# Kernel tuning notes

Hardware: AMD Instinct MI355X
Metric: run time of the kernel (lower is better)

The kernel has to match this reference:

```python
import jax, jax.numpy as jnp
import numpy as np
from jax.scipy.linalg import expm as _expm

B, D = 1024, 128
_SQRT3 = 3.0 ** 0.5
_C1, _C2 = 0.5 - _SQRT3 / 6.0, 0.5 + _SQRT3 / 6.0


def setup_inputs() -> dict:
    key = jax.random.key(0)
    k_t, k_y, k_a, k_w = jax.random.split(key, 4)
    scale = 1.0 / np.sqrt(D)  # keep ||Omega|| moderate so expm is well-conditioned
    return {
        "t0": jax.random.uniform(k_t, (B,), dtype=jnp.float32),
        "h": jnp.float32(0.1),
        "y0": jax.random.normal(k_y, (B, D), dtype=jnp.float32),
        "A0": jax.random.normal(k_a, (B, D, D), dtype=jnp.float32) * scale,
        "W": jax.random.normal(k_w, (B, D, D), dtype=jnp.float32) * scale,
    }


def reference(t0, h, y0, A0, W):
    # A(t) = A0 + t * W evaluated at the two Gauss-Legendre nodes
    t1 = t0 + _C1 * h  # (B,)
    t2 = t0 + _C2 * h  # (B,)
    A1 = A0 + t1[:, None, None] * W  # (B, D, D)
    A2 = A0 + t2[:, None, None] * W  # (B, D, D)
    alpha1 = (h * 0.5) * (A1 + A2)
    alpha2 = (h * _SQRT3) * (A2 - A1)
    comm = alpha1 @ alpha2 - alpha2 @ alpha1  # [alpha1, alpha2]
    Omega = alpha1 - comm / 12.0
    U = jax.vmap(_expm)(Omega)  # batched matrix exponential (B, D, D)
    y_next = jnp.einsum("bij,bj->bi", U, y0)  # (B, D)
    return y_next, jnp.stack((A1, A2), axis=0)
```

## Files before the change

kernel.cpp:

```cpp
#include <hip/hip_runtime.h>

#define B_SZ 1024
#define D_SZ 128
#define KTERMS 7
#define QPAD 36

typedef float vfloat4 __attribute__((ext_vector_type(4)));

__device__ inline float bflo(unsigned u) { return __uint_as_float(u << 16); }
__device__ inline float bfhi(unsigned u) { return __uint_as_float(u & 0xffff0000u); }

__device__ inline void dot32x2(const unsigned* ra, const unsigned* rw,
                               const float* v, float& oa, float& ow) {
    float a0=0.f,a1=0.f,a2=0.f,a3=0.f, w0=0.f,w1=0.f,w2=0.f,w3=0.f;
#pragma unroll
    for (int j = 0; j < 8; ++j) {
        vfloat4 vv = *(const vfloat4*)(v + 4 * j);
        a0 = fmaf(bflo(ra[2*j]),   vv.x, a0);
        a1 = fmaf(bfhi(ra[2*j]),   vv.y, a1);
        a2 = fmaf(bflo(ra[2*j+1]), vv.z, a2);
        a3 = fmaf(bfhi(ra[2*j+1]), vv.w, a3);
        w0 = fmaf(bflo(rw[2*j]),   vv.x, w0);
        w1 = fmaf(bfhi(rw[2*j]),   vv.y, w1);
        w2 = fmaf(bflo(rw[2*j+1]), vv.z, w2);
        w3 = fmaf(bfhi(rw[2*j+1]), vv.w, w3);
    }
    oa = (a0 + a1) + (a2 + a3);
    ow = (w0 + w1) + (w2 + w3);
}

__device__ inline float dot32(const unsigned* rq, const float* v) {
    float a0=0.f,a1=0.f,a2=0.f,a3=0.f;
#pragma unroll
    for (int j = 0; j < 8; ++j) {
        vfloat4 vv = *(const vfloat4*)(v + 4 * j);
        a0 = fmaf(bflo(rq[2*j]),   vv.x, a0);
        a1 = fmaf(bfhi(rq[2*j]),   vv.y, a1);
        a2 = fmaf(bflo(rq[2*j+1]), vv.z, a2);
        a3 = fmaf(bfhi(rq[2*j+1]), vv.w, a3);
    }
    return (a0 + a1) + (a2 + a3);
}

__global__ void __launch_bounds__(512, 4)
magnus_kernel(const float* __restrict__ t0p, const float* __restrict__ hp,
              const float* __restrict__ y0, const float* __restrict__ A0,
              const float* __restrict__ W, float* __restrict__ out)
{
    __shared__ __align__(16) float svr [4 * QPAD];
    __shared__ __align__(16) float su1r[4 * QPAD];
    __shared__ __align__(16) float su2r[4 * QPAD];

    const int b   = blockIdx.x;
    const int tid = threadIdx.x;
    const int row = tid >> 2;
    const int q   = tid & 3;
    const float h  = hp[0];
    const float tb = t0p[b];
    const float SQ3_6 = 0.28867513459481287f;
    const float t1 = tb + (0.5f - SQ3_6) * h;
    const float t2 = tb + (0.5f + SQ3_6) * h;

    const size_t moff = (size_t)b * (D_SZ * D_SZ);

    const int fbase = row * 32 + q * 8;
    const float4* Ap = (const float4*)(A0 + moff) + fbase;
    const float4* Wp = (const float4*)(W + moff) + fbase;
    float4 ta[8], tw[8];
#pragma unroll
    for (int it = 0; it < 8; ++it) { ta[it] = Ap[it]; tw[it] = Wp[it]; }
    float yv = y0[(size_t)b * D_SZ + row];

    {
        const float4* A0v = (const float4*)(A0 + moff);
        const float4* Wv  = (const float4*)(W + moff);
        vfloat4* o1 = (vfloat4*)(out + (size_t)B_SZ * D_SZ + moff);
        vfloat4* o2 = (vfloat4*)(out + (size_t)B_SZ * D_SZ
                                     + (size_t)B_SZ * D_SZ * D_SZ + moff);
#pragma unroll 8
        for (int it = 0; it < 8; ++it) {
            int i = it * 512 + tid;
            float4 a = A0v[i];
            float4 w = Wv[i];
            vfloat4 p1, p2;
            p1.x = fmaf(t1, w.x, a.x); p1.y = fmaf(t1, w.y, a.y);
            p1.z = fmaf(t1, w.z, a.z); p1.w = fmaf(t1, w.w, a.w);
            p2.x = fmaf(t2, w.x, a.x); p2.y = fmaf(t2, w.y, a.y);
            p2.z = fmaf(t2, w.z, a.z); p2.w = fmaf(t2, w.w, a.w);
            __builtin_nontemporal_store(p1, o1 + i);
            __builtin_nontemporal_store(p2, o2 + i);
        }
    }

    unsigned ra[16], rw[16];
#pragma unroll
    for (int it = 0; it < 8; ++it) {
        asm("v_cvt_pk_bf16_f32 %0, %1, %2" : "=v"(ra[2*it])   : "v"(ta[it].x), "v"(ta[it].y));
        asm("v_cvt_pk_bf16_f32 %0, %1, %2" : "=v"(ra[2*it+1]) : "v"(ta[it].z), "v"(ta[it].w));
        asm("v_cvt_pk_bf16_f32 %0, %1, %2" : "=v"(rw[2*it])   : "v"(tw[it].x), "v"(tw[it].y));
        asm("v_cvt_pk_bf16_f32 %0, %1, %2" : "=v"(rw[2*it+1]) : "v"(tw[it].z), "v"(tw[it].w));
    }

    float yacc = yv;
    if (tid < D_SZ) {
        svr[(tid >> 5) * QPAD + (tid & 31)] = y0[(size_t)b * D_SZ + tid];
    }
    __syncthreads();

    const float hs = h * (tb + 0.5f * h);
    const float c3 = h * h * h * (1.0f / 12.0f);
    const int uflat = (row >> 5) * QPAD + (row & 31);

#pragma unroll
    for (int k = 1; k <= KTERMS; ++k) {
        float pa, pw;
        dot32x2(ra, rw, svr + q * QPAD, pa, pw);
        pa += __shfl_xor(pa, 1); pa += __shfl_xor(pa, 2);
        pw += __shfl_xor(pw, 1); pw += __shfl_xor(pw, 2);
        if (q == 0) { su1r[uflat] = pa; su2r[uflat] = pw; }
        __syncthreads();
        float pb = dot32(ra, su2r + q * QPAD);
        float pc = dot32(rw, su1r + q * QPAD);
        pb += __shfl_xor(pb, 1); pb += __shfl_xor(pb, 2);
        pc += __shfl_xor(pc, 1); pc += __shfl_xor(pc, 2);
        float wn = (h * pa + hs * pw - c3 * (pb - pc)) * (1.0f / (float)k);
        yacc += wn;
        if (k < KTERMS) {
            if (q == 0) svr[uflat] = wn;
            __syncthreads();
        }
    }

    if (q == 0) {
        out[(size_t)b * D_SZ + row] = yacc;
    }
}

extern "C" void kernel_launch(void* const* d_in, const int* in_sizes, int n_in,
                              void* d_out, int out_size, void* d_ws, size_t ws_size,
                              hipStream_t stream) {
    const float* t0 = (const float*)d_in[0];
    const float* h  = (const float*)d_in[1];
    const float* y0 = (const float*)d_in[2];
    const float* A0 = (const float*)d_in[3];
    const float* W  = (const float*)d_in[4];
    float* out = (float*)d_out;
    magnus_kernel<<<B_SZ, 512, 0, stream>>>(t0, h, y0, A0, W, out);
}
```

Baseline: 264.5 us.

## Split each batch into separate A1/A2 writer and Magnus-solve blocks via atomic job queue

Launches twice as many blocks and uses per-CU atomic tickets to assign each block either the A1/A2 output-writing job or the Krylov-style exponential-action job for a batch item. Job selection alternates per compute unit (keyed off hardware and XCC IDs), so the bandwidth-bound store work and the latency-bound iterative matvec work are meant to co-reside and overlap. The cost is reading A0/W twice, an extra memset, and atomic contention, plus relying on non-portable hardware register reads.

```diff
diff --git a/kernel.cpp b/kernel.cpp
--- a/kernel.cpp
+++ b/kernel.cpp
@@ -4,6 +4,7 @@
 #define D_SZ 128
 #define KTERMS 7
 #define QPAD 36
+#define NSLOT 2048
 
 typedef float vfloat4 __attribute__((ext_vector_type(4)));
 
@@ -45,33 +46,44 @@
 __global__ void __launch_bounds__(512, 4)
 magnus_kernel(const float* __restrict__ t0p, const float* __restrict__ hp,
               const float* __restrict__ y0, const float* __restrict__ A0,
-              const float* __restrict__ W, float* __restrict__ out)
+              const float* __restrict__ W, float* __restrict__ out,
+              int* __restrict__ ws)
 {
     __shared__ __align__(16) float svr [4 * QPAD];
     __shared__ __align__(16) float su1r[4 * QPAD];
     __shared__ __align__(16) float su2r[4 * QPAD];
+    __shared__ int sjob, sb;
 
-    const int b   = blockIdx.x;
     const int tid = threadIdx.x;
-    const int row = tid >> 2;
-    const int q   = tid & 3;
+
+    if (tid == 0) {
+        unsigned hwid, xcc;
+        asm volatile("s_getreg_b32 %0, hwreg(HW_REG_HW_ID)" : "=s"(hwid));
+        asm volatile("s_getreg_b32 %0, hwreg(HW_REG_XCC_ID)" : "=s"(xcc));
+        int slot = ((xcc & 7) << 8) | ((hwid >> 8) & 0xFF);
+        int ticket = atomicAdd(&ws[slot], 1);
+        int job = ticket & 1;
+        int b = atomicAdd(&ws[NSLOT + job], 1);
+        if (b >= B_SZ) {
+            job ^= 1;
+            b = atomicAdd(&ws[NSLOT + job], 1);
+        }
+        sjob = job;
+        sb = (b < B_SZ) ? b : -1;
+    }
+    __syncthreads();
+    const int job = sjob;
+    const int b = sb;
+    if (b < 0) return;
+
     const float h  = hp[0];
     const float tb = t0p[b];
-    const float SQ3_6 = 0.28867513459481287f;
-    const float t1 = tb + (0.5f - SQ3_6) * h;
-    const float t2 = tb + (0.5f + SQ3_6) * h;
-
     const size_t moff = (size_t)b * (D_SZ * D_SZ);
 
-    const int fbase = row * 32 + q * 8;
-    const float4* Ap = (const float4*)(A0 + moff) + fbase;
-    const float4* Wp = (const float4*)(W + moff) + fbase;
-    float4 ta[8], tw[8];
-#pragma unroll
-    for (int it = 0; it < 8; ++it) { ta[it] = Ap[it]; tw[it] = Wp[it]; }
-    float yv = y0[(size_t)b * D_SZ + row];
-
-    {
+    if (job == 0) {
+        const float SQ3_6 = 0.28867513459481287f;
+        const float t1 = tb + (0.5f - SQ3_6) * h;
+        const float t2 = tb + (0.5f + SQ3_6) * h;
         const float4* A0v = (const float4*)(A0 + moff);
         const float4* Wv  = (const float4*)(W + moff);
         vfloat4* o1 = (vfloat4*)(out + (size_t)B_SZ * D_SZ + moff);
@@ -90,18 +102,27 @@
             __builtin_nontemporal_store(p1, o1 + i);
             __builtin_nontemporal_store(p2, o2 + i);
         }
+        return;
     }
 
+    const int row = tid >> 2;
+    const int q   = tid & 3;
+    const int fbase = row * 32 + q * 8;
+
+    const float4* Ap = (const float4*)(A0 + moff) + fbase;
+    const float4* Wp = (const float4*)(W + moff) + fbase;
     unsigned ra[16], rw[16];
 #pragma unroll
     for (int it = 0; it < 8; ++it) {
-        asm("v_cvt_pk_bf16_f32 %0, %1, %2" : "=v"(ra[2*it])   : "v"(ta[it].x), "v"(ta[it].y));
-        asm("v_cvt_pk_bf16_f32 %0, %1, %2" : "=v"(ra[2*it+1]) : "v"(ta[it].z), "v"(ta[it].w));
-        asm("v_cvt_pk_bf16_f32 %0, %1, %2" : "=v"(rw[2*it])   : "v"(tw[it].x), "v"(tw[it].y));
-        asm("v_cvt_pk_bf16_f32 %0, %1, %2" : "=v"(rw[2*it+1]) : "v"(tw[it].z), "v"(tw[it].w));
+        float4 a = Ap[it];
+        float4 w = Wp[it];
+        asm("v_cvt_pk_bf16_f32 %0, %1, %2" : "=v"(ra[2*it])   : "v"(a.x), "v"(a.y));
+        asm("v_cvt_pk_bf16_f32 %0, %1, %2" : "=v"(ra[2*it+1]) : "v"(a.z), "v"(a.w));
+        asm("v_cvt_pk_bf16_f32 %0, %1, %2" : "=v"(rw[2*it])   : "v"(w.x), "v"(w.y));
+        asm("v_cvt_pk_bf16_f32 %0, %1, %2" : "=v"(rw[2*it+1]) : "v"(w.z), "v"(w.w));
     }
 
-    float yacc = yv;
+    float yacc = y0[(size_t)b * D_SZ + row];
     if (tid < D_SZ) {
         svr[(tid >> 5) * QPAD + (tid & 31)] = y0[(size_t)b * D_SZ + tid];
     }
@@ -145,5 +166,7 @@
     const float* A0 = (const float*)d_in[3];
     const float* W  = (const float*)d_in[4];
     float* out = (float*)d_out;
-    magnus_kernel<<<B_SZ, 512, 0, stream>>>(t0, h, y0, A0, W, out);
+    hipMemsetAsync(d_ws, 0, (NSLOT + 2) * sizeof(int), stream);
+    magnus_kernel<<<2 * B_SZ, 512, 0, stream>>>(t0, h, y0, A0, W, out,
+                                                (int*)d_ws);
 }
```

Result: no change. 269.7 us (+2.0%).
